# Optimization experiments

Hardware: AMD Instinct MI355X
Metric: run time of the kernel (lower is better)

Reference implementation:

```python
import jax, jax.numpy as jnp
import numpy as np

B, D, H1, H2 = 512, 1024, 512, 128

def setup_inputs() -> dict:
    key = jax.random.key(0)
    ks = jax.random.split(key, 3)
    x = jax.random.normal(ks[0], (B, D), dtype=jnp.float32)
    W1 = jax.random.normal(ks[1], (H1, D), dtype=jnp.float32)
    W2 = jax.random.normal(ks[2], (H2, H1), dtype=jnp.float32)
    b1 = jnp.full((H1,), 0.1, dtype=jnp.float32)
    b2 = jnp.full((H2,), 0.1, dtype=jnp.float32)
    b3 = jnp.full((H1,), 0.1, dtype=jnp.float32)
    b_r = jnp.full((D,), 0.1, dtype=jnp.float32)
    return {"x": x, "W1": W1, "b1": b1, "W2": W2, "b2": b2, "b3": b3, "b_r": b_r}

def reference(x, W1, b1, W2, b2, b3, b_r):
    # encoder
    c1 = jax.nn.sigmoid(x @ W1.T + b1)          # [B, H1]
    c2 = jax.nn.sigmoid(c1 @ W2.T + b2)         # [B, H2]
    # decoder (tied weights)
    c3 = jax.nn.sigmoid(c2 @ W2 + b3)           # [B, H1]
    recover = c3 @ W1 + b_r                     # [B, D]
    # Jacobian of code w.r.t. x, batched (replaces per-sample diag+matmul loop):
    # Jac[b] = diag(c2'(b)) @ W2 @ diag(c1'(b)) @ W1
    s1p = c1 * (1.0 - c1)                       # [B, H1]
    s2p = c2 * (1.0 - c2)                       # [B, H2]
    M = s2p[:, :, None] * W2[None, :, :] * s1p[:, None, :]   # [B, H2, H1]
    Jac = jnp.einsum('bhk,kd->bhd', M, W1)      # [B, H2, D]
    return (recover, c2, Jac)
```

## Files before the change

kernel.cpp:

```cpp
#include <hip/hip_runtime.h>


typedef _Float16 f16x8 __attribute__((ext_vector_type(8)));
typedef _Float16 f16x4 __attribute__((ext_vector_type(4)));
typedef float    f32x4 __attribute__((ext_vector_type(4)));
typedef float    f32x2 __attribute__((ext_vector_type(2)));

__device__ __forceinline__ void gld_lds16(const _Float16* src, _Float16* dst_wave_uniform) {
    __builtin_amdgcn_global_load_lds((const __attribute__((address_space(1))) unsigned int*)src,
                                     (__attribute__((address_space(3))) unsigned int*)dst_wave_uniform,
                                     16, 0, 0);
}

__global__ __launch_bounds__(256) void prep_kernel(const float* __restrict__ W1,
                                                   const float* __restrict__ W2,
                                                   _Float16* __restrict__ W1T,
                                                   _Float16* __restrict__ W2h) {
    int bx = blockIdx.x;
    if (bx < 512) {
        __shared__ float tile[32][33];
        int dt = (bx & 31) * 32, kt = (bx >> 5) * 32;
        int tx = threadIdx.x & 31, ty = threadIdx.x >> 5;
        #pragma unroll
        for (int r = 0; r < 32; r += 8)
            tile[ty + r][tx] = W1[(kt + ty + r) * 1024 + dt + tx];
        __syncthreads();
        #pragma unroll
        for (int r = 0; r < 32; r += 8)
            W1T[(size_t)(dt + ty + r) * 512 + kt + tx] = (_Float16)tile[tx][ty + r];
    } else {
        int i = (bx - 512) * 1024 + threadIdx.x * 4;
        f32x4 v = *(const f32x4*)(W2 + i);
        f16x4 h;
        h.x = (_Float16)v.x; h.y = (_Float16)v.y; h.z = (_Float16)v.z; h.w = (_Float16)v.w;
        *(f16x4*)(W2h + i) = h;
    }
}

template <int EPI, bool TRANSB>
__global__ __launch_bounds__(256) void gemm_f32(const float* __restrict__ A,
                                                const float* __restrict__ Bm,
                                                const float* __restrict__ bias,
                                                float* __restrict__ C,
                                                float* __restrict__ Cd,
                                                _Float16* __restrict__ Ch,
                                                int M, int N, int K) {
    __shared__ __align__(16) float As[16][34];
    __shared__ __align__(16) float Bs[16][68];
    const int n0 = blockIdx.x * 64, m0 = blockIdx.y * 32;
    const int tid = threadIdx.x, tx = tid & 15, ty = tid >> 4;
    float acc[2][4] = {};

    for (int k0 = 0; k0 < K; k0 += 16) {
        #pragma unroll
        for (int r = 0; r < 2; ++r) {
            int m = (tid >> 4) + r * 16, k = tid & 15;
            As[k][m] = A[(size_t)(m0 + m) * K + k0 + k];
        }
        if (TRANSB) {
            #pragma unroll
            for (int r = 0; r < 4; ++r) {
                int n = (tid >> 4) + r * 16, k = tid & 15;
                Bs[k][n] = Bm[(size_t)(n0 + n) * K + k0 + k];
            }
        } else {
            #pragma unroll
            for (int r = 0; r < 4; ++r) {
                int k = (tid >> 6) + r * 4, n = tid & 63;
                Bs[k][n] = Bm[(size_t)(k0 + k) * N + n0 + n];
            }
        }
        __syncthreads();
        #pragma unroll
        for (int k = 0; k < 16; ++k) {
            f32x2 av = *(const f32x2*)&As[k][ty * 2];
            f32x4 bv = *(const f32x4*)&Bs[k][tx * 4];
            #pragma unroll
            for (int i = 0; i < 2; ++i)
                #pragma unroll
                for (int j = 0; j < 4; ++j)
                    acc[i][j] += av[i] * bv[j];
        }
        __syncthreads();
    }

    #pragma unroll
    for (int i = 0; i < 2; ++i) {
        int row = m0 + ty * 2 + i;
        #pragma unroll
        for (int j = 0; j < 4; ++j) {
            int col = n0 + tx * 4 + j;
            float z = acc[i][j] + bias[col];
            float s = 1.f / (1.f + __expf(-z));
            if constexpr (EPI == 1) {
                C[(size_t)row * N + col]  = s;
                Cd[(size_t)row * N + col] = s * (1.f - s);
            } else {
                Ch[(size_t)row * N + col] = (_Float16)s;
            }
        }
    }
}

__global__ __launch_bounds__(256) void build_A(const float* __restrict__ W2,
                                               const float* __restrict__ s1p,
                                               const float* __restrict__ s2p,
                                               _Float16* __restrict__ A_all) {
    const int b = blockIdx.x, tid = threadIdx.x;
    __shared__ float S1[512];
    __shared__ float S2[128];
    S1[tid]       = s1p[(size_t)b * 512 + tid];
    S1[tid + 256] = s1p[(size_t)b * 512 + tid + 256];
    if (tid < 128) S2[tid] = s2p[(size_t)b * 128 + tid];
    __syncthreads();
    _Float16* out = A_all + (size_t)b * 65536;
    #pragma unroll 4
    for (int i = 0; i < 32; ++i) {
        int c = tid + 256 * i;
        int h = c >> 6, k8 = (c & 63) * 8;
        f32x4 w0 = *(const f32x4*)(W2 + h * 512 + k8);
        f32x4 w1 = *(const f32x4*)(W2 + h * 512 + k8 + 4);
        float s2 = S2[h];
        f16x8 o;
        o[0] = (_Float16)(s2 * w0.x * S1[k8 + 0]);
        o[1] = (_Float16)(s2 * w0.y * S1[k8 + 1]);
        o[2] = (_Float16)(s2 * w0.z * S1[k8 + 2]);
        o[3] = (_Float16)(s2 * w0.w * S1[k8 + 3]);
        o[4] = (_Float16)(s2 * w1.x * S1[k8 + 4]);
        o[5] = (_Float16)(s2 * w1.y * S1[k8 + 5]);
        o[6] = (_Float16)(s2 * w1.z * S1[k8 + 6]);
        o[7] = (_Float16)(s2 * w1.w * S1[k8 + 7]);
        *(f16x8*)(out + h * 512 + k8) = o;
    }
}

template <bool HAS_BIAS>
__global__ __launch_bounds__(256) void mfma_bt(const _Float16* __restrict__ Abase,
                                               const _Float16* __restrict__ Bmat,
                                               const float* __restrict__ bias,
                                               float* __restrict__ OutBase,
                                               int K, int N,
                                               long aBatch, long oBatch) {
    __shared__ __align__(16) _Float16 Asl[128 * 64];
    __shared__ __align__(16) _Float16 Bsl[128 * 64];
    __shared__ float Bias[128];
    const _Float16* A = Abase + (size_t)blockIdx.z * aBatch;
    float* Out = OutBase + (size_t)blockIdx.z * oBatch;
    const int m0 = blockIdx.y * 128, n0 = blockIdx.x * 128;
    const int tid = threadIdx.x;
    const int lane = tid & 63, wave = tid >> 6;
    const int wm = (wave >> 1) * 64, wn = (wave & 1) * 64;
    const int l15 = lane & 15, q = lane >> 4;

    if (HAS_BIAS && tid < 128) Bias[tid] = bias[n0 + tid];

    f32x4 acc[4][4];
    #pragma unroll
    for (int i = 0; i < 4; ++i)
        #pragma unroll
        for (int j = 0; j < 4; ++j) acc[i][j] = (f32x4){0.f, 0.f, 0.f, 0.f};

    const int rbase = wave * 8 + (lane >> 3);
    const int kof   = (lane & 7) * 8;

    for (int k0 = 0; k0 < K; k0 += 64) {
        #pragma unroll
        for (int r = 0; r < 4; ++r) {
            gld_lds16(A    + (size_t)(m0 + r * 32 + rbase) * K + k0 + kof, Asl + (r * 32 + wave * 8) * 64);
            gld_lds16(Bmat + (size_t)(n0 + r * 32 + rbase) * K + k0 + kof, Bsl + (r * 32 + wave * 8) * 64);
        }
        __syncthreads();
        #pragma unroll
        for (int kk = 0; kk < 64; kk += 32) {
            f16x8 af[4], bf[4];
            #pragma unroll
            for (int i = 0; i < 4; ++i)
                af[i] = *(const f16x8*)(Asl + (wm + i * 16 + l15) * 64 + kk + q * 8);
            #pragma unroll
            for (int j = 0; j < 4; ++j)
                bf[j] = *(const f16x8*)(Bsl + (wn + j * 16 + l15) * 64 + kk + q * 8);
            #pragma unroll
            for (int i = 0; i < 4; ++i)
                #pragma unroll
                for (int j = 0; j < 4; ++j)
                    acc[i][j] = __builtin_amdgcn_mfma_f32_16x16x32_f16(af[i], bf[j], acc[i][j], 0, 0, 0);
        }
        __syncthreads();
    }

    #pragma unroll
    for (int i = 0; i < 4; ++i) {
        #pragma unroll
        for (int rg = 0; rg < 4; ++rg) {
            int m = m0 + wm + i * 16 + q * 4 + rg;
            #pragma unroll
            for (int j = 0; j < 4; ++j) {
                int dcol = wn + j * 16 + l15;
                float v = acc[i][j][rg];
                if (HAS_BIAS) v += Bias[dcol];
                Out[(size_t)m * N + n0 + dcol] = v;
            }
        }
    }
}

__global__ __launch_bounds__(256) void jac_kernel(const _Float16* __restrict__ W2h,
                                                  const _Float16* __restrict__ W1T,
                                                  const float* __restrict__ s1p,
                                                  const float* __restrict__ s2p,
                                                  float* __restrict__ Jac) {
    __shared__ __align__(16) _Float16 Asl[128 * 64];
    __shared__ __align__(16) _Float16 Bsl[128 * 64];
    __shared__ float Ssl[128];
    const int b  = blockIdx.y;
    const int n0 = blockIdx.x * 128;
    const int tid = threadIdx.x;
    const int lane = tid & 63, wave = tid >> 6;
    const int wm = (wave >> 1) * 64, wn = (wave & 1) * 64;
    const int l15 = lane & 15, q = lane >> 4;

    if (tid < 128) Ssl[tid] = s2p[b * 128 + tid];

    f32x4 acc[4][4];
    #pragma unroll
    for (int i = 0; i < 4; ++i)
        #pragma unroll
        for (int j = 0; j < 4; ++j) acc[i][j] = (f32x4){0.f, 0.f, 0.f, 0.f};

    const int ah  = tid >> 4;
    const int akq = (tid & 15) * 4;
    const int rbase = wave * 8 + (lane >> 3);
    const int kof   = (lane & 7) * 8;

    for (int k0 = 0; k0 < 512; k0 += 64) {
        f32x4 s4 = *(const f32x4*)(s1p + (size_t)b * 512 + k0 + akq);
        f16x4 s4h;
        s4h.x = (_Float16)s4.x; s4h.y = (_Float16)s4.y;
        s4h.z = (_Float16)s4.z; s4h.w = (_Float16)s4.w;
        #pragma unroll
        for (int r = 0; r < 8; ++r) {
            int h = ah + r * 16;
            f16x4 w4 = *(const f16x4*)(W2h + (size_t)h * 512 + k0 + akq);
            *(f16x4*)(Asl + h * 64 + akq) = w4 * s4h;
        }
        #pragma unroll
        for (int r = 0; r < 4; ++r)
            gld_lds16(W1T + (size_t)(n0 + r * 32 + rbase) * 512 + k0 + kof,
                      Bsl + (r * 32 + wave * 8) * 64);
        __syncthreads();

        #pragma unroll
        for (int kk = 0; kk < 64; kk += 32) {
            f16x8 af[4], bf[4];
            #pragma unroll
            for (int i = 0; i < 4; ++i)
                af[i] = *(const f16x8*)(Asl + (wm + i * 16 + l15) * 64 + kk + q * 8);
            #pragma unroll
            for (int j = 0; j < 4; ++j)
                bf[j] = *(const f16x8*)(Bsl + (wn + j * 16 + l15) * 64 + kk + q * 8);
            #pragma unroll
            for (int i = 0; i < 4; ++i)
                #pragma unroll
                for (int j = 0; j < 4; ++j)
                    acc[i][j] = __builtin_amdgcn_mfma_f32_16x16x32_f16(af[i], bf[j], acc[i][j], 0, 0, 0);
        }
        __syncthreads();
    }

    float* outb = Jac + (size_t)b * (128 * 1024);
    #pragma unroll
    for (int i = 0; i < 4; ++i) {
        #pragma unroll
        for (int rg = 0; rg < 4; ++rg) {
            int h = wm + i * 16 + q * 4 + rg;
            float s = Ssl[h];
            #pragma unroll
            for (int j = 0; j < 4; ++j) {
                int d = n0 + wn + j * 16 + l15;
                outb[(size_t)h * 1024 + d] = acc[i][j][rg] * s;
            }
        }
    }
}

extern "C" void kernel_launch(void* const* d_in, const int* in_sizes, int n_in,
                              void* d_out, int out_size, void* d_ws, size_t ws_size,
                              hipStream_t stream) {
    const float* x  = (const float*)d_in[0];
    const float* W1 = (const float*)d_in[1];
    const float* b1 = (const float*)d_in[2];
    const float* W2 = (const float*)d_in[3];
    const float* b2 = (const float*)d_in[4];
    const float* b3 = (const float*)d_in[5];
    const float* br = (const float*)d_in[6];

    float* out_rec = (float*)d_out;
    float* out_c2  = out_rec + 512 * 1024;
    float* out_jac = out_c2 + 512 * 128;

    char* ws = (char*)d_ws;
    _Float16* W1T   = (_Float16*)(ws);
    _Float16* W2h   = (_Float16*)(ws + 0x100000);
    float*    c1    = (float*)(ws + 0x120000);
    float*    s1p   = (float*)(ws + 0x220000);
    float*    s2p   = (float*)(ws + 0x320000);
    _Float16* c3h   = (_Float16*)(ws + 0x360000);
    _Float16* A_all = (_Float16*)(ws + 0x400000);
    const bool big_ws = ws_size >= (size_t)0x4400000;

    prep_kernel<<<576, 256, 0, stream>>>(W1, W2, W1T, W2h);
    gemm_f32<1, true ><<<dim3(8, 16), 256, 0, stream>>>(x,      W1, b1, c1,     s1p, nullptr, 512, 512, 1024);
    gemm_f32<1, true ><<<dim3(2, 16), 256, 0, stream>>>(c1,     W2, b2, out_c2, s2p, nullptr, 512, 128, 512);
    gemm_f32<2, false><<<dim3(8, 16), 256, 0, stream>>>(out_c2, W2, b3, nullptr, nullptr, c3h, 512, 512, 128);
    mfma_bt<true><<<dim3(8, 4, 1), 256, 0, stream>>>(c3h, W1T, br, out_rec, 512, 1024, 0, 0);
    if (big_ws) {
        build_A<<<512, 256, 0, stream>>>(W2, s1p, s2p, A_all);
        mfma_bt<false><<<dim3(8, 1, 512), 256, 0, stream>>>(A_all, W1T, nullptr, out_jac,
                                                            512, 1024, 65536, 131072);
    } else {
        jac_kernel<<<dim3(8, 512), 256, 0, stream>>>(W2h, W1T, s1p, s2p, out_jac);
    }
}
```

Before: 460.4 us.

## Replace fp32 encoder GEMMs with split-fp16 MFMA and widen Jacobian tiles

The three scalar fp32 encoder/decoder GEMMs become MFMA GEMMs. The first two emulate fp32 accuracy by splitting operands into hi/lo fp16 parts and concatenating them along K (hi*hi + hi*lo + lo*hi). The prep kernel now also produces these split copies plus a transposed fp16 W2. The batched Jacobian GEMM becomes a dedicated 256x128-tile kernel that covers two samples per block, which raises data reuse of W1T. The cost is extra prep traffic, a tripled K in the split GEMMs, and higher register and LDS pressure in the Jacobian kernel.

After: 480.1 us. 1.04x slower.

```diff
diff --git a/kernel.cpp b/kernel.cpp
--- a/kernel.cpp
+++ b/kernel.cpp
@@ -4,7 +4,6 @@
 typedef _Float16 f16x8 __attribute__((ext_vector_type(8)));
 typedef _Float16 f16x4 __attribute__((ext_vector_type(4)));
 typedef float    f32x4 __attribute__((ext_vector_type(4)));
-typedef float    f32x2 __attribute__((ext_vector_type(2)));
 
 __device__ __forceinline__ void gld_lds16(const _Float16* src, _Float16* dst_wave_uniform) {
     __builtin_amdgcn_global_load_lds((const __attribute__((address_space(1))) unsigned int*)src,
@@ -14,13 +13,18 @@
 
 __global__ __launch_bounds__(256) void prep_kernel(const float* __restrict__ W1,
                                                    const float* __restrict__ W2,
+                                                   const float* __restrict__ x,
                                                    _Float16* __restrict__ W1T,
-                                                   _Float16* __restrict__ W2h) {
-    int bx = blockIdx.x;
+                                                   _Float16* __restrict__ W2h,
+                                                   _Float16* __restrict__ W2T_h,
+                                                   _Float16* __restrict__ W1s,
+                                                   _Float16* __restrict__ xs,
+                                                   _Float16* __restrict__ W2s) {
+    int bx = blockIdx.x, tid = threadIdx.x;
     if (bx < 512) {
         __shared__ float tile[32][33];
         int dt = (bx & 31) * 32, kt = (bx >> 5) * 32;
-        int tx = threadIdx.x & 31, ty = threadIdx.x >> 5;
+        int tx = tid & 31, ty = tid >> 5;
         #pragma unroll
         for (int r = 0; r < 32; r += 8)
             tile[ty + r][tx] = W1[(kt + ty + r) * 1024 + dt + tx];
@@ -28,75 +32,125 @@
         #pragma unroll
         for (int r = 0; r < 32; r += 8)
             W1T[(size_t)(dt + ty + r) * 512 + kt + tx] = (_Float16)tile[tx][ty + r];
-    } else {
-        int i = (bx - 512) * 1024 + threadIdx.x * 4;
+    } else if (bx < 576) {
+        int i = (bx - 512) * 1024 + tid * 4;
         f32x4 v = *(const f32x4*)(W2 + i);
         f16x4 h;
         h.x = (_Float16)v.x; h.y = (_Float16)v.y; h.z = (_Float16)v.z; h.w = (_Float16)v.w;
         *(f16x4*)(W2h + i) = h;
-    }
-}
-
-template <int EPI, bool TRANSB>
-__global__ __launch_bounds__(256) void gemm_f32(const float* __restrict__ A,
-                                                const float* __restrict__ Bm,
-                                                const float* __restrict__ bias,
-                                                float* __restrict__ C,
-                                                float* __restrict__ Cd,
-                                                _Float16* __restrict__ Ch,
-                                                int M, int N, int K) {
-    __shared__ __align__(16) float As[16][34];
-    __shared__ __align__(16) float Bs[16][68];
-    const int n0 = blockIdx.x * 64, m0 = blockIdx.y * 32;
-    const int tid = threadIdx.x, tx = tid & 15, ty = tid >> 4;
-    float acc[2][4] = {};
-
-    for (int k0 = 0; k0 < K; k0 += 16) {
-        #pragma unroll
-        for (int r = 0; r < 2; ++r) {
-            int m = (tid >> 4) + r * 16, k = tid & 15;
-            As[k][m] = A[(size_t)(m0 + m) * K + k0 + k];
-        }
-        if (TRANSB) {
-            #pragma unroll
-            for (int r = 0; r < 4; ++r) {
-                int n = (tid >> 4) + r * 16, k = tid & 15;
-                Bs[k][n] = Bm[(size_t)(n0 + n) * K + k0 + k];
-            }
-        } else {
-            #pragma unroll
-            for (int r = 0; r < 4; ++r) {
-                int k = (tid >> 6) + r * 4, n = tid & 63;
-                Bs[k][n] = Bm[(size_t)(k0 + k) * N + n0 + n];
-            }
-        }
-        __syncthreads();
-        #pragma unroll
-        for (int k = 0; k < 16; ++k) {
-            f32x2 av = *(const f32x2*)&As[k][ty * 2];
-            f32x4 bv = *(const f32x4*)&Bs[k][tx * 4];
+    } else if (bx < 640) {
+        __shared__ float tile[32][33];
+        int t = bx - 576;
+        int kt = (t & 3) * 32, nt = (t >> 2) * 32;
+        int tx = tid & 31, ty = tid >> 5;
+        #pragma unroll
+        for (int r = 0; r < 32; r += 8)
+            tile[ty + r][tx] = W2[(kt + ty + r) * 512 + nt + tx];
+        __syncthreads();
+        #pragma unroll
+        for (int r = 0; r < 32; r += 8)
+            W2T_h[(size_t)(nt + ty + r) * 128 + kt + tx] = (_Float16)tile[tx][ty + r];
+    } else if (bx < 1152) {
+        int t = bx - 640, col = tid * 4;
+        f32x4 v = *(const f32x4*)(W1 + (size_t)t * 1024 + col);
+        f16x4 h, l;
+        #pragma unroll
+        for (int i = 0; i < 4; ++i) { h[i] = (_Float16)v[i]; l[i] = (_Float16)(v[i] - (float)h[i]); }
+        _Float16* row = W1s + (size_t)t * 3072;
+        *(f16x4*)(row + col) = h;
+        *(f16x4*)(row + 1024 + col) = l;
+        *(f16x4*)(row + 2048 + col) = h;
+    } else if (bx < 1664) {
+        int t = bx - 1152, col = tid * 4;
+        f32x4 v = *(const f32x4*)(x + (size_t)t * 1024 + col);
+        f16x4 h, l;
+        #pragma unroll
+        for (int i = 0; i < 4; ++i) { h[i] = (_Float16)v[i]; l[i] = (_Float16)(v[i] - (float)h[i]); }
+        _Float16* row = xs + (size_t)t * 3072;
+        *(f16x4*)(row + col) = h;
+        *(f16x4*)(row + 1024 + col) = h;
+        *(f16x4*)(row + 2048 + col) = l;
+    } else {
+        int t = bx - 1664;
+        int row = t * 2 + (tid >> 7), col = (tid & 127) * 4;
+        f32x4 v = *(const f32x4*)(W2 + (size_t)row * 512 + col);
+        f16x4 h, l;
+        #pragma unroll
+        for (int i = 0; i < 4; ++i) { h[i] = (_Float16)v[i]; l[i] = (_Float16)(v[i] - (float)h[i]); }
+        _Float16* orow = W2s + (size_t)row * 1536;
+        *(f16x4*)(orow + col) = h;
+        *(f16x4*)(orow + 512 + col) = l;
+        *(f16x4*)(orow + 1024 + col) = h;
+    }
+}
+
+template <int EPI>
+__global__ __launch_bounds__(64) void sgemm(const _Float16* __restrict__ A,
+                                            const _Float16* __restrict__ B,
+                                            const float* __restrict__ bias,
+                                            int K,
+                                            float* __restrict__ o1,
+                                            float* __restrict__ o2,
+                                            _Float16* __restrict__ o3) {
+    __shared__ __align__(16) _Float16 As[32 * 64];
+    __shared__ __align__(16) _Float16 Bs[32 * 64];
+    const int m0 = blockIdx.y * 32, n0 = blockIdx.x * 32;
+    const int lane = threadIdx.x;
+    const int l15 = lane & 15, q = lane >> 4;
+    const int rrow = lane >> 3, kof = (lane & 7) * 8;
+
+    f32x4 acc[2][2];
+    #pragma unroll
+    for (int i = 0; i < 2; ++i)
+        #pragma unroll
+        for (int j = 0; j < 2; ++j) acc[i][j] = (f32x4){0.f, 0.f, 0.f, 0.f};
+
+    for (int k0 = 0; k0 < K; k0 += 64) {
+        #pragma unroll
+        for (int r = 0; r < 4; ++r) {
+            gld_lds16(A + (size_t)(m0 + r * 8 + rrow) * K + k0 + kof, As + r * 512);
+            gld_lds16(B + (size_t)(n0 + r * 8 + rrow) * K + k0 + kof, Bs + r * 512);
+        }
+        __syncthreads();
+        #pragma unroll
+        for (int kk = 0; kk < 64; kk += 32) {
+            f16x8 af[2], bf[2];
+            #pragma unroll
+            for (int i = 0; i < 2; ++i) af[i] = *(const f16x8*)(As + (i * 16 + l15) * 64 + kk + q * 8);
+            #pragma unroll
+            for (int j = 0; j < 2; ++j) bf[j] = *(const f16x8*)(Bs + (j * 16 + l15) * 64 + kk + q * 8);
             #pragma unroll
             for (int i = 0; i < 2; ++i)
                 #pragma unroll
-                for (int j = 0; j < 4; ++j)
-                    acc[i][j] += av[i] * bv[j];
+                for (int j = 0; j < 2; ++j)
+                    acc[i][j] = __builtin_amdgcn_mfma_f32_16x16x32_f16(af[i], bf[j], acc[i][j], 0, 0, 0);
         }
         __syncthreads();
     }
 
     #pragma unroll
     for (int i = 0; i < 2; ++i) {
-        int row = m0 + ty * 2 + i;
-        #pragma unroll
-        for (int j = 0; j < 4; ++j) {
-            int col = n0 + tx * 4 + j;
-            float z = acc[i][j] + bias[col];
-            float s = 1.f / (1.f + __expf(-z));
-            if constexpr (EPI == 1) {
-                C[(size_t)row * N + col]  = s;
-                Cd[(size_t)row * N + col] = s * (1.f - s);
-            } else {
-                Ch[(size_t)row * N + col] = (_Float16)s;
+        #pragma unroll
+        for (int rg = 0; rg < 4; ++rg) {
+            int row = m0 + i * 16 + q * 4 + rg;
+            #pragma unroll
+            for (int j = 0; j < 2; ++j) {
+                int col = n0 + j * 16 + l15;
+                float z = acc[i][j][rg] + bias[col];
+                float s = 1.f / (1.f + __expf(-z));
+                if constexpr (EPI == 0) {
+                    _Float16 h = (_Float16)s;
+                    _Float16 lo = (_Float16)(s - (float)h);
+                    _Float16* rp = o3 + (size_t)row * 1536;
+                    rp[col] = h; rp[512 + col] = h; rp[1024 + col] = lo;
+                    o2[(size_t)row * 512 + col] = s * (1.f - s);
+                } else if constexpr (EPI == 1) {
+                    o1[(size_t)row * 128 + col] = s;
+                    o2[(size_t)row * 128 + col] = s * (1.f - s);
+                    o3[(size_t)row * 128 + col] = (_Float16)s;
+                } else {
+                    o3[(size_t)row * 512 + col] = (_Float16)s;
+                }
             }
         }
     }
@@ -135,17 +189,14 @@
 }
 
 template <bool HAS_BIAS>
-__global__ __launch_bounds__(256) void mfma_bt(const _Float16* __restrict__ Abase,
+__global__ __launch_bounds__(256) void mfma_bt(const _Float16* __restrict__ A,
                                                const _Float16* __restrict__ Bmat,
                                                const float* __restrict__ bias,
-                                               float* __restrict__ OutBase,
-                                               int K, int N,
-                                               long aBatch, long oBatch) {
+                                               float* __restrict__ Out,
+                                               int K, int N) {
     __shared__ __align__(16) _Float16 Asl[128 * 64];
     __shared__ __align__(16) _Float16 Bsl[128 * 64];
     __shared__ float Bias[128];
-    const _Float16* A = Abase + (size_t)blockIdx.z * aBatch;
-    float* Out = OutBase + (size_t)blockIdx.z * oBatch;
     const int m0 = blockIdx.y * 128, n0 = blockIdx.x * 128;
     const int tid = threadIdx.x;
     const int lane = tid & 63, wave = tid >> 6;
@@ -199,6 +250,67 @@
                 float v = acc[i][j][rg];
                 if (HAS_BIAS) v += Bias[dcol];
                 Out[(size_t)m * N + n0 + dcol] = v;
+            }
+        }
+    }
+}
+
+__global__ __launch_bounds__(256) void jac256(const _Float16* __restrict__ A_all,
+                                              const _Float16* __restrict__ W1T,
+                                              float* __restrict__ Jac) {
+    __shared__ __align__(16) _Float16 Asl[256 * 64];
+    __shared__ __align__(16) _Float16 Bsl[128 * 64];
+    const int n0 = blockIdx.x * 128;
+    const _Float16* A = A_all + (size_t)blockIdx.y * 131072;
+    float* Out = Jac + (size_t)blockIdx.y * 262144;
+    const int tid = threadIdx.x;
+    const int lane = tid & 63, wave = tid >> 6;
+    const int wm = wave * 64;
+    const int l15 = lane & 15, q = lane >> 4;
+    const int rbase = wave * 8 + (lane >> 3);
+    const int kof   = (lane & 7) * 8;
+
+    f32x4 acc[4][8];
+    #pragma unroll
+    for (int i = 0; i < 4; ++i)
+        #pragma unroll
+        for (int j = 0; j < 8; ++j) acc[i][j] = (f32x4){0.f, 0.f, 0.f, 0.f};
+
+    for (int k0 = 0; k0 < 512; k0 += 64) {
+        #pragma unroll
+        for (int r = 0; r < 8; ++r)
+            gld_lds16(A + (size_t)(r * 32 + rbase) * 512 + k0 + kof, Asl + (r * 32 + wave * 8) * 64);
+        #pragma unroll
+        for (int r = 0; r < 4; ++r)
+            gld_lds16(W1T + (size_t)(n0 + r * 32 + rbase) * 512 + k0 + kof, Bsl + (r * 32 + wave * 8) * 64);
+        __syncthreads();
+        #pragma unroll
+        for (int kk = 0; kk < 64; kk += 32) {
+            f16x8 af[4], bf[8];
+            #pragma unroll
+            for (int i = 0; i < 4; ++i)
+                af[i] = *(const f16x8*)(Asl + (wm + i * 16 + l15) * 64 + kk + q * 8);
+            #pragma unroll
+            for (int j = 0; j < 8; ++j)
+                bf[j] = *(const f16x8*)(Bsl + (j * 16 + l15) * 64 + kk + q * 8);
+            #pragma unroll
+            for (int i = 0; i < 4; ++i)
+                #pragma unroll
+                for (int j = 0; j < 8; ++j)
+                    acc[i][j] = __builtin_amdgcn_mfma_f32_16x16x32_f16(af[i], bf[j], acc[i][j], 0, 0, 0);
+        }
+        __syncthreads();
+    }
+
+    #pragma unroll
+    for (int i = 0; i < 4; ++i) {
+        #pragma unroll
+        for (int rg = 0; rg < 4; ++rg) {
+            int m = wm + i * 16 + q * 4 + rg;
+            #pragma unroll
+            for (int j = 0; j < 8; ++j) {
+                int d = n0 + j * 16 + l15;
+                Out[(size_t)m * 1024 + d] = acc[i][j][rg];
             }
         }
     }
@@ -301,22 +413,26 @@
     char* ws = (char*)d_ws;
     _Float16* W1T   = (_Float16*)(ws);
     _Float16* W2h   = (_Float16*)(ws + 0x100000);
-    float*    c1    = (float*)(ws + 0x120000);
-    float*    s1p   = (float*)(ws + 0x220000);
-    float*    s2p   = (float*)(ws + 0x320000);
-    _Float16* c3h   = (_Float16*)(ws + 0x360000);
-    _Float16* A_all = (_Float16*)(ws + 0x400000);
-    const bool big_ws = ws_size >= (size_t)0x4400000;
-
-    prep_kernel<<<576, 256, 0, stream>>>(W1, W2, W1T, W2h);
-    gemm_f32<1, true ><<<dim3(8, 16), 256, 0, stream>>>(x,      W1, b1, c1,     s1p, nullptr, 512, 512, 1024);
-    gemm_f32<1, true ><<<dim3(2, 16), 256, 0, stream>>>(c1,     W2, b2, out_c2, s2p, nullptr, 512, 128, 512);
-    gemm_f32<2, false><<<dim3(8, 16), 256, 0, stream>>>(out_c2, W2, b3, nullptr, nullptr, c3h, 512, 512, 128);
-    mfma_bt<true><<<dim3(8, 4, 1), 256, 0, stream>>>(c3h, W1T, br, out_rec, 512, 1024, 0, 0);
+    _Float16* W2T_h = (_Float16*)(ws + 0x120000);
+    _Float16* c1s   = (_Float16*)(ws + 0x140000);
+    float*    s1p   = (float*)   (ws + 0x2C0000);
+    float*    s2p   = (float*)   (ws + 0x3C0000);
+    _Float16* c2h   = (_Float16*)(ws + 0x400000);
+    _Float16* c3h   = (_Float16*)(ws + 0x420000);
+    _Float16* W1s   = (_Float16*)(ws + 0x4A0000);
+    _Float16* xs    = (_Float16*)(ws + 0x7A0000);
+    _Float16* W2s   = (_Float16*)(ws + 0xAA0000);
+    _Float16* A_all = (_Float16*)(ws + 0xB00000);
+    const bool big_ws = ws_size >= (size_t)0x4B00000;
+
+    prep_kernel<<<1728, 256, 0, stream>>>(W1, W2, x, W1T, W2h, W2T_h, W1s, xs, W2s);
+    sgemm<0><<<dim3(16, 16), 64, 0, stream>>>(xs, W1s, b1, 3072, nullptr, s1p, c1s);
+    sgemm<1><<<dim3(4, 16), 64, 0, stream>>>(c1s, W2s, b2, 1536, out_c2, s2p, c2h);
+    sgemm<2><<<dim3(16, 16), 64, 0, stream>>>(c2h, W2T_h, b3, 128, nullptr, nullptr, c3h);
+    mfma_bt<true><<<dim3(8, 4), 256, 0, stream>>>(c3h, W1T, br, out_rec, 512, 1024);
     if (big_ws) {
         build_A<<<512, 256, 0, stream>>>(W2, s1p, s2p, A_all);
-        mfma_bt<false><<<dim3(8, 1, 512), 256, 0, stream>>>(A_all, W1T, nullptr, out_jac,
-                                                            512, 1024, 65536, 131072);
+        jac256<<<dim3(8, 256), 256, 0, stream>>>(A_all, W1T, out_jac);
     } else {
         jac_kernel<<<dim3(8, 512), 256, 0, stream>>>(W2h, W1T, s1p, s2p, out_jac);
     }
```
